# Optimization experiments

Hardware: AMD Instinct MI355X
Metric: run time of the kernel (lower is better)

Reference implementation:

```python
import jax, jax.numpy as jnp
import numpy as np

B, T, L = 4096, 26, 4      # batch, num sparse tables, bag size (multi-hot)
N_ROWS, M = 100000, 64     # rows per table, embedding dim
LN_BOT = [13, 512, 256, 64]
LN_TOP = [415, 512, 256, 1]


def _mlp_params(key, ln):
    Ws, bs = [], []
    for i in range(len(ln) - 1):
        n, m = ln[i], ln[i + 1]
        key, k1, k2 = jax.random.split(key, 3)
        Ws.append(jax.random.normal(k1, (m, n), jnp.float32) * np.sqrt(2.0 / (m + n)))
        bs.append(jax.random.normal(k2, (m,), jnp.float32) * np.sqrt(1.0 / m))
    return Ws, bs


def setup_inputs() -> dict:
    key = jax.random.key(0)
    k_dense, k_idx, k_emb, k_bot, k_top = jax.random.split(key, 5)
    dense_x = jax.random.normal(k_dense, (B, LN_BOT[0]), jnp.float32)
    sparse_idx = jax.random.randint(k_idx, (B, T, L), 0, N_ROWS, jnp.int64 if jax.config.jax_enable_x64 else jnp.int32)
    # per-table uniform init U(-1/sqrt(n), 1/sqrt(n)); all tables same size -> stacked
    bound = np.sqrt(1.0 / N_ROWS)
    emb_tables = jax.random.uniform(k_emb, (T, N_ROWS, M), jnp.float32, -bound, bound)
    bw, bb = _mlp_params(k_bot, LN_BOT)
    tw, tb = _mlp_params(k_top, LN_TOP)
    return {
        "dense_x": dense_x, "sparse_idx": sparse_idx, "emb_tables": emb_tables,
        "bot_W0": bw[0], "bot_b0": bb[0], "bot_W1": bw[1], "bot_b1": bb[1],
        "bot_W2": bw[2], "bot_b2": bb[2],
        "top_W0": tw[0], "top_b0": tb[0], "top_W1": tw[1], "top_b1": tb[1],
        "top_W2": tw[2], "top_b2": tb[2],
    }


def _dlrm_forward(dense_x, sparse_idx, emb_tables, bot, top):
    # bottom MLP (all ReLU; sigmoid_layer index not hit for bottom)
    x = dense_x
    for W, b in bot:
        x = jax.nn.relu(x @ W.T + b)                       # [B, 64] at the end
    # apply_emb: per-table EmbeddingBag(mode='sum'): gather L rows, sum-pool
    # emb_tables: [T, N, M], sparse_idx: [B, T, L] -> E: [B, T, M]
    E = jax.vmap(lambda tab, ix: tab[ix].sum(axis=1), in_axes=(0, 1), out_axes=1)(
        emb_tables, sparse_idx)
    # dot interaction: concat bottom output with pooled embeddings
    Tcat = jnp.concatenate([x[:, None, :], E], axis=1)     # [B, T+1, M]
    Z = jnp.einsum("bim,bjm->bij", Tcat, Tcat)             # [B, T+1, T+1]
    li, lj = np.tril_indices(T + 1, k=-1)                  # strictly lower triangle
    Zflat = Z[:, li, lj]                                   # [B, (T+1)T/2]
    R = jnp.concatenate([x, Zflat], axis=1)                # [B, 415]
    # top MLP: ReLU hidden, Sigmoid on last layer
    h = R
    for i, (W, b) in enumerate(top):
        h = h @ W.T + b
        h = jax.nn.sigmoid(h) if i == len(top) - 1 else jax.nn.relu(h)
    return h                                               # [B, 1]


def reference(dense_x, sparse_idx, emb_tables,
              bot_W0, bot_b0, bot_W1, bot_b1, bot_W2, bot_b2,
              top_W0, top_b0, top_W1, top_b1, top_W2, top_b2):
    bot = [(bot_W0, bot_b0), (bot_W1, bot_b1), (bot_W2, bot_b2)]
    top = [(top_W0, top_b0), (top_W1, top_b1), (top_W2, top_b2)]
    return _dlrm_forward(dense_x, sparse_idx, emb_tables, bot, top)
```

## Files before the change

kernel.cpp:

```cpp
#include <hip/hip_runtime.h>
#include <hip/hip_bf16.h>
#include <cstddef>
#include <cstdint>

#define BATCH 4096
#define TT 26
#define LL 4
#define NROWS 100000
#define MM 64
#define RSTR 512

typedef __attribute__((ext_vector_type(8))) short bf16x8;
typedef __attribute__((ext_vector_type(4))) float f32x4;

#define AS1 __attribute__((address_space(1)))
#define AS3 __attribute__((address_space(3)))

__device__ __forceinline__ void gload_lds16(const void* g, void* l) {
    __builtin_amdgcn_global_load_lds((const AS1 unsigned int*)g,
                                     (AS3 unsigned int*)l, 16, 0, 0);
}

__device__ __forceinline__ float bu2f(unsigned short u) {
    unsigned int x = (unsigned int)u << 16;
    float f; __builtin_memcpy(&f, &x, 4); return f;
}

#define CONV_BLOCKS 2112
__global__ __launch_bounds__(256) void prep_kernel(
    const float* __restrict__ dense, const float* __restrict__ bw0,
    const float* __restrict__ bb0,
    const float* __restrict__ bw1, const float* __restrict__ bw2,
    const float* __restrict__ tw0, const float* __restrict__ tw1,
    __hip_bfloat16* __restrict__ x1,
    __hip_bfloat16* __restrict__ bw1b, __hip_bfloat16* __restrict__ bw2b,
    __hip_bfloat16* __restrict__ tw0b, __hip_bfloat16* __restrict__ tw1b)
{
    __shared__ float xr[13];
    if (blockIdx.x < CONV_BLOCKS) {
        int i = blockIdx.x * 256 + threadIdx.x;
        if (i < 131072) {
            bw1b[i] = __float2bfloat16(bw1[i]);
        } else if (i < 147456) {
            int j = i - 131072; bw2b[j] = __float2bfloat16(bw2[j]);
        } else if (i < 409600) {
            int j = i - 147456; int n = j >> 9, k = j & 511;
            tw0b[j] = __float2bfloat16(k < 415 ? tw0[n * 415 + k] : 0.f);
        } else {
            int j = i - 409600; tw1b[j] = __float2bfloat16(tw1[j]);
        }
        return;
    }
    int b = blockIdx.x - CONV_BLOCKS;
    if (threadIdx.x < 13) xr[threadIdx.x] = dense[b * 13 + threadIdx.x];
    __syncthreads();
    for (int j = threadIdx.x; j < 512; j += 256) {
        const float* w = bw0 + j * 13;
        float s = bb0[j];
#pragma unroll
        for (int k = 0; k < 13; k++) s = fmaf(xr[k], w[k], s);
        x1[(size_t)b * 512 + j] = __float2bfloat16(fmaxf(s, 0.f));
    }
}

template<int KK, int ACT>
__global__ __launch_bounds__(256) void gemm_fullk(
    const __hip_bfloat16* __restrict__ A,
    const __hip_bfloat16* __restrict__ W,
    const float* __restrict__ bias,
    __hip_bfloat16* __restrict__ C, int ldc)
{
    constexpr int HS   = KK / 2;
    constexpr int CPRH = KK / 16;
    constexpr int NI   = (64 * CPRH) / 256;
    __shared__ __align__(16) short As0[64 * HS];
    __shared__ __align__(16) short As1[64 * HS];
    __shared__ __align__(16) short Bs0[64 * HS];
    __shared__ __align__(16) short Bs1[64 * HS];

    const int tid  = threadIdx.x;
    const int lane = tid & 63;
    const int wid  = tid >> 6;
    const int wr   = wid >> 1, wc = wid & 1;

    const char* Ab = (const char*)A + (size_t)blockIdx.x * (64 * KK * 2);
    const char* Wb = (const char*)W + (size_t)blockIdx.y * (64 * KK * 2);

    auto stage = [&](const char* Gb, short* Ls, int h) {
#pragma unroll
        for (int j = 0; j < NI; j++) {
            int ci  = j * 256 + tid;
            int row = ci / CPRH;
            int cb  = (ci & (CPRH - 1)) * 16;
            int src = row * (2 * KK) + h * KK + (cb ^ ((row & 7) << 4));
            gload_lds16(Gb + src, (char*)Ls + row * KK + cb);
        }
    };
    stage(Ab, As0, 0); stage(Wb, Bs0, 0);
    stage(Ab, As1, 1); stage(Wb, Bs1, 1);

    const int frow = lane & 15;
    const int fkb  = (lane >> 4) * 16;
    const int xr   = (frow & 7) << 4;
    const int oA0  = (wr * 32 + frow) * KK;
    const int oA1  = oA0 + 16 * KK;
    const int oB0  = (wc * 32 + frow) * KK;
    const int oB1  = oB0 + 16 * KK;

    f32x4 acc[2][2] = {};

    auto compute = [&](const short* Ah, const short* Bh) {
#pragma unroll
        for (int ks = 0; ks < KK / 64; ks++) {
            int pc = (ks * 64 + fkb) ^ xr;
            bf16x8 a0 = *(const bf16x8*)((const char*)Ah + oA0 + pc);
            bf16x8 a1 = *(const bf16x8*)((const char*)Ah + oA1 + pc);
            bf16x8 b0 = *(const bf16x8*)((const char*)Bh + oB0 + pc);
            bf16x8 b1 = *(const bf16x8*)((const char*)Bh + oB1 + pc);
            acc[0][0] = __builtin_amdgcn_mfma_f32_16x16x32_bf16(a0, b0, acc[0][0], 0, 0, 0);
            acc[0][1] = __builtin_amdgcn_mfma_f32_16x16x32_bf16(a0, b1, acc[0][1], 0, 0, 0);
            acc[1][0] = __builtin_amdgcn_mfma_f32_16x16x32_bf16(a1, b0, acc[1][0], 0, 0, 0);
            acc[1][1] = __builtin_amdgcn_mfma_f32_16x16x32_bf16(a1, b1, acc[1][1], 0, 0, 0);
        }
    };

    asm volatile("s_waitcnt vmcnt(%0)" :: "i"(2 * NI) : "memory");
    __builtin_amdgcn_sched_barrier(0);
    __builtin_amdgcn_s_barrier();
    __builtin_amdgcn_sched_barrier(0);
    compute(As0, Bs0);
    asm volatile("s_waitcnt vmcnt(0)" ::: "memory");
    __builtin_amdgcn_sched_barrier(0);
    __builtin_amdgcn_s_barrier();
    __builtin_amdgcn_sched_barrier(0);
    compute(As1, Bs1);

    const int col0 = blockIdx.y * 64 + wc * 32 + (lane & 15);
    const int row0 = blockIdx.x * 64 + wr * 32 + (lane >> 4) * 4;
    float bias_n0 = bias[col0];
    float bias_n1 = bias[col0 + 16];
#pragma unroll
    for (int mi = 0; mi < 2; mi++) {
#pragma unroll
        for (int j = 0; j < 4; j++) {
            int row = row0 + mi * 16 + j;
            float v0 = acc[mi][0][j] + bias_n0;
            float v1 = acc[mi][1][j] + bias_n1;
            if (ACT == 1) { v0 = fmaxf(v0, 0.f); v1 = fmaxf(v1, 0.f); }
            C[(size_t)row * ldc + col0]      = __float2bfloat16(v0);
            C[(size_t)row * ldc + col0 + 16] = __float2bfloat16(v1);
        }
    }
}

__global__ __launch_bounds__(256) void embed_interact_kernel(
    const int* __restrict__ idx, const float* __restrict__ emb,
    __hip_bfloat16* __restrict__ R)
{
    __shared__ float S[27 * 68];
    __shared__ int sidx[TT * LL];
    const int b = blockIdx.x;
    const int tid = threadIdx.x;
    const int lane = tid & 63;
    const int wid = tid >> 6;

    if (tid < TT * LL) sidx[tid] = idx[(size_t)b * (TT * LL) + tid];
    __syncthreads();

    float v[7][4];
#pragma unroll
    for (int rr = 0; rr < 7; rr++) {
        const int r = rr * 4 + wid;
        if (r == 0) {
            v[rr][0] = __bfloat162float(R[(size_t)b * RSTR + lane]);
            v[rr][1] = 0.f; v[rr][2] = 0.f; v[rr][3] = 0.f;
        } else if (r < 27) {
            const int t = r - 1;
            const float* tab = emb + (size_t)t * NROWS * MM;
#pragma unroll
            for (int l = 0; l < LL; l++)
                v[rr][l] = tab[(size_t)sidx[t * LL + l] * MM + lane];
        }
    }
#pragma unroll
    for (int rr = 0; rr < 7; rr++) {
        const int r = rr * 4 + wid;
        if (r < 27) S[r * 68 + lane] = v[rr][0] + v[rr][1] + v[rr][2] + v[rr][3];
    }
    __syncthreads();

    __hip_bfloat16* Rb = R + (size_t)b * RSTR;
    if (tid < 97) Rb[415 + tid] = __float2bfloat16(0.f);
    for (int e = tid; e < 351; e += 256) {
        int i = (int)((1.0f + sqrtf(1.0f + 8.0f * (float)e)) * 0.5f);
        while (i * (i - 1) / 2 > e) i--;
        while ((i + 1) * i / 2 <= e) i++;
        int j = e - i * (i - 1) / 2;
        const float* si_ = &S[i * 68];
        const float* sj_ = &S[j * 68];
        float s = 0.f;
#pragma unroll
        for (int k = 0; k < 16; k++) {
            float4 a  = *(const float4*)&si_[k * 4];
            float4 c4 = *(const float4*)&sj_[k * 4];
            s += a.x * c4.x + a.y * c4.y + a.z * c4.z + a.w * c4.w;
        }
        Rb[64 + e] = __float2bfloat16(s);
    }
}

__global__ __launch_bounds__(256) void top2_kernel(
    const __hip_bfloat16* __restrict__ h, const float* __restrict__ W,
    const float* __restrict__ bias, float* __restrict__ out)
{
    __shared__ float ws[256];
    int tid = threadIdx.x;
    ws[tid] = W[tid];
    __syncthreads();
    int b = blockIdx.x * 4 + (tid >> 6);
    int lane = tid & 63;
    const unsigned short* hb = (const unsigned short*)(h + (size_t)b * 256);
    ushort4 hv = *(const ushort4*)&hb[lane * 4];
    float4 wv = *(const float4*)&ws[lane * 4];
    float s = bu2f(hv.x) * wv.x + bu2f(hv.y) * wv.y + bu2f(hv.z) * wv.z + bu2f(hv.w) * wv.w;
#pragma unroll
    for (int off = 32; off >= 1; off >>= 1)
        s += __shfl_xor(s, off, 64);
    if (lane == 0) {
        float v = s + bias[0];
        out[b] = 1.0f / (1.0f + expf(-v));
    }
}

extern "C" void kernel_launch(void* const* d_in, const int* in_sizes, int n_in,
                              void* d_out, int out_size, void* d_ws, size_t ws_size,
                              hipStream_t stream) {
    const float* dense = (const float*)d_in[0];
    const int*   sidx  = (const int*)d_in[1];
    const float* emb   = (const float*)d_in[2];
    const float* bw0   = (const float*)d_in[3];
    const float* bb0   = (const float*)d_in[4];
    const float* bw1   = (const float*)d_in[5];
    const float* bb1   = (const float*)d_in[6];
    const float* bw2   = (const float*)d_in[7];
    const float* bb2   = (const float*)d_in[8];
    const float* tw0   = (const float*)d_in[9];
    const float* tb0   = (const float*)d_in[10];
    const float* tw1   = (const float*)d_in[11];
    const float* tb1   = (const float*)d_in[12];
    const float* tw2   = (const float*)d_in[13];
    const float* tb2   = (const float*)d_in[14];
    float* out = (float*)d_out;

    char* wsb = (char*)d_ws;
    __hip_bfloat16* x1   = (__hip_bfloat16*)(wsb);
    __hip_bfloat16* x2   = (__hip_bfloat16*)(wsb + (4u << 20));
    __hip_bfloat16* R    = (__hip_bfloat16*)(wsb + (8u << 20));
    __hip_bfloat16* h1   = (__hip_bfloat16*)(wsb + (12u << 20));
    __hip_bfloat16* h2   = (__hip_bfloat16*)(wsb + (16u << 20));
    __hip_bfloat16* bw1b = (__hip_bfloat16*)(wsb + (18u << 20));
    __hip_bfloat16* bw2b = bw1b + 131072;
    __hip_bfloat16* tw0b = bw2b + 16384;
    __hip_bfloat16* tw1b = tw0b + 262144;

    prep_kernel<<<CONV_BLOCKS + BATCH, 256, 0, stream>>>(
        dense, bw0, bb0, bw1, bw2, tw0, tw1, x1, bw1b, bw2b, tw0b, tw1b);

    gemm_fullk<512, 1><<<dim3(64, 4), 256, 0, stream>>>(x1, bw1b, bb1, x2, 256);

    gemm_fullk<256, 1><<<dim3(64, 1), 256, 0, stream>>>(x2, bw2b, bb2, R, RSTR);

    embed_interact_kernel<<<BATCH, 256, 0, stream>>>(sidx, emb, R);

    gemm_fullk<512, 1><<<dim3(64, 8), 256, 0, stream>>>(R, tw0b, tb0, h1, 512);

    gemm_fullk<512, 1><<<dim3(64, 4), 256, 0, stream>>>(h1, tw1b, tb1, h2, 256);

    top2_kernel<<<BATCH / 4, 256, 0, stream>>>(h2, tw2, tb2, out);
}
```

Measured before the change: 55.66 us.

## Fuse bottom MLP last layer into embedding gather and MFMA interaction kernel

Removes the separate last bottom-MLP GEMM launch by computing it inside the embedding kernel with 16x16x32 bf16 MFMA for 4 batch rows per block. Each wave now handles one sample, storing pooled embeddings as bf16 in a swizzled LDS tile, and computes the 27x27 Gram matrix with 32x32x16 MFMAs instead of scalar dot products with triangular index decoding. This saves a launch and the scalar interaction work, but rounds pooled embeddings to bf16 before the dot products. The MFMA operand mapping for the tiny GEMM (only 4 real rows in a 16-row tile) wastes lanes.

```diff
diff --git a/kernel.cpp b/kernel.cpp
--- a/kernel.cpp
+++ b/kernel.cpp
@@ -12,6 +12,7 @@
 
 typedef __attribute__((ext_vector_type(8))) short bf16x8;
 typedef __attribute__((ext_vector_type(4))) float f32x4;
+typedef __attribute__((ext_vector_type(16))) float f32x16;
 
 #define AS1 __attribute__((address_space(1)))
 #define AS3 __attribute__((address_space(3)))
@@ -153,59 +154,88 @@
     }
 }
 
-__global__ __launch_bounds__(256) void embed_interact_kernel(
+__global__ __launch_bounds__(256) void bot2_embed_interact(
     const int* __restrict__ idx, const float* __restrict__ emb,
-    __hip_bfloat16* __restrict__ R)
+    const __hip_bfloat16* __restrict__ x2, const __hip_bfloat16* __restrict__ w2b,
+    const float* __restrict__ bb2, __hip_bfloat16* __restrict__ R)
 {
-    __shared__ float S[27 * 68];
-    __shared__ int sidx[TT * LL];
-    const int b = blockIdx.x;
-    const int tid = threadIdx.x;
+    __shared__ __align__(16) short T[4][32 * 64];
+    __shared__ int sidx[4 * TT * LL];
+    const int tid  = threadIdx.x;
     const int lane = tid & 63;
-    const int wid = tid >> 6;
-
-    if (tid < TT * LL) sidx[tid] = idx[(size_t)b * (TT * LL) + tid];
+    const int w    = tid >> 6;
+    const int b0   = blockIdx.x * 4;
+
+    for (int i = tid; i < 4 * TT * LL; i += 256)
+        sidx[i] = idx[(size_t)b0 * (TT * LL) + i];
+
+    {
+        f32x4 acc = {};
+        const short* xg = (const short*)x2 + (size_t)(b0 + (lane & 3)) * 256 + (lane >> 4) * 8;
+        const short* wg = (const short*)w2b + (size_t)(w * 16 + (lane & 15)) * 256 + (lane >> 4) * 8;
+#pragma unroll
+        for (int ks = 0; ks < 8; ks++) {
+            bf16x8 a  = *(const bf16x8*)(xg + ks * 32);
+            bf16x8 bf = *(const bf16x8*)(wg + ks * 32);
+            acc = __builtin_amdgcn_mfma_f32_16x16x32_bf16(a, bf, acc, 0, 0, 0);
+        }
+        __syncthreads();
+        if (lane < 16) {
+            int col = w * 16 + lane;
+            float bias = bb2[col];
+#pragma unroll
+            for (int j = 0; j < 4; j++) {
+                float v = fmaxf(acc[j] + bias, 0.f);
+                __hip_bfloat16 hv = __float2bfloat16(v);
+                R[(size_t)(b0 + j) * RSTR + col] = hv;
+                T[j][col] = *(short*)&hv;
+            }
+        }
+    }
+
+#pragma unroll
+    for (int r = 27; r < 32; r++) {
+        int byteoff = r * 128 + ((lane * 2) ^ ((r & 7) << 4));
+        *(short*)((char*)T[w] + byteoff) = 0;
+    }
+
+#pragma unroll
+    for (int t = 0; t < TT; t++) {
+        const float* tab = emb + (size_t)t * NROWS * MM + lane;
+        const int* ip = &sidx[(w * TT + t) * LL];
+        float s = tab[(size_t)ip[0] * MM] + tab[(size_t)ip[1] * MM]
+                + tab[(size_t)ip[2] * MM] + tab[(size_t)ip[3] * MM];
+        __hip_bfloat16 hv = __float2bfloat16(s);
+        int r = t + 1;
+        int byteoff = r * 128 + ((lane * 2) ^ ((r & 7) << 4));
+        *(short*)((char*)T[w] + byteoff) = *(short*)&hv;
+    }
     __syncthreads();
 
-    float v[7][4];
-#pragma unroll
-    for (int rr = 0; rr < 7; rr++) {
-        const int r = rr * 4 + wid;
-        if (r == 0) {
-            v[rr][0] = __bfloat162float(R[(size_t)b * RSTR + lane]);
-            v[rr][1] = 0.f; v[rr][2] = 0.f; v[rr][3] = 0.f;
-        } else if (r < 27) {
-            const int t = r - 1;
-            const float* tab = emb + (size_t)t * NROWS * MM;
-#pragma unroll
-            for (int l = 0; l < LL; l++)
-                v[rr][l] = tab[(size_t)sidx[t * LL + l] * MM + lane];
-        }
-    }
-#pragma unroll
-    for (int rr = 0; rr < 7; rr++) {
-        const int r = rr * 4 + wid;
-        if (r < 27) S[r * 68 + lane] = v[rr][0] + v[rr][1] + v[rr][2] + v[rr][3];
-    }
-    __syncthreads();
-
-    __hip_bfloat16* Rb = R + (size_t)b * RSTR;
-    if (tid < 97) Rb[415 + tid] = __float2bfloat16(0.f);
-    for (int e = tid; e < 351; e += 256) {
-        int i = (int)((1.0f + sqrtf(1.0f + 8.0f * (float)e)) * 0.5f);
-        while (i * (i - 1) / 2 > e) i--;
-        while ((i + 1) * i / 2 <= e) i++;
-        int j = e - i * (i - 1) / 2;
-        const float* si_ = &S[i * 68];
-        const float* sj_ = &S[j * 68];
-        float s = 0.f;
-#pragma unroll
-        for (int k = 0; k < 16; k++) {
-            float4 a  = *(const float4*)&si_[k * 4];
-            float4 c4 = *(const float4*)&sj_[k * 4];
-            s += a.x * c4.x + a.y * c4.y + a.z * c4.z + a.w * c4.w;
-        }
-        Rb[64 + e] = __float2bfloat16(s);
+    {
+        f32x16 acc = {};
+#pragma unroll
+        for (int m = 0; m < 4; m++) {
+            int byteoff = (lane & 31) * 128 +
+                          ((m * 32 + (lane >> 5) * 16) ^ (((lane & 31) & 7) << 4));
+            bf16x8 f = *(const bf16x8*)((const char*)T[w] + byteoff);
+            acc = __builtin_amdgcn_mfma_f32_32x32x16_bf16(f, f, acc, 0, 0, 0);
+        }
+        __hip_bfloat16* Rb = R + (size_t)(b0 + w) * RSTR;
+        const int col = lane & 31;
+#pragma unroll
+        for (int q = 0; q < 4; q++) {
+#pragma unroll
+            for (int j = 0; j < 4; j++) {
+                int row = j + 8 * q + 4 * (lane >> 5);
+                if (row < 27 && col < row) {
+                    int e = row * (row - 1) / 2 + col;
+                    Rb[64 + e] = __float2bfloat16(acc[q * 4 + j]);
+                }
+            }
+        }
+        for (int p = lane; p < 97; p += 64)
+            Rb[415 + p] = __float2bfloat16(0.f);
     }
 }
 
@@ -268,9 +298,7 @@
 
     gemm_fullk<512, 1><<<dim3(64, 4), 256, 0, stream>>>(x1, bw1b, bb1, x2, 256);
 
-    gemm_fullk<256, 1><<<dim3(64, 1), 256, 0, stream>>>(x2, bw2b, bb2, R, RSTR);
-
-    embed_interact_kernel<<<BATCH, 256, 0, stream>>>(sidx, emb, R);
+    bot2_embed_interact<<<BATCH / 4, 256, 0, stream>>>(sidx, emb, x2, bw2b, bb2, R);
 
     gemm_fullk<512, 1><<<dim3(64, 8), 256, 0, stream>>>(R, tw0b, tb0, h1, 512);
 
```

After: 63.64 us. 1.14x slower.

## Compute embedding dot interactions with a single-wave bf16 MFMA Gram matrix

Applied to the files above, without the earlier changes.

Pooled embeddings are stored to LDS as bf16 in a XOR-swizzled 32x64 tile, with padding rows zeroed. One wavefront then computes the full 32x32 Gram matrix with four 32x32x16 bf16 MFMAs and writes out the strictly lower triangle. This replaces the per-thread scalar fp32 dot products and the triangular index search. It lowers the precision of the interaction inputs to bf16, and only one wave does the interaction while the other three sit idle.

```diff
diff --git a/kernel.cpp b/kernel.cpp
--- a/kernel.cpp
+++ b/kernel.cpp
@@ -12,6 +12,7 @@
 
 typedef __attribute__((ext_vector_type(8))) short bf16x8;
 typedef __attribute__((ext_vector_type(4))) float f32x4;
+typedef __attribute__((ext_vector_type(16))) float f32x16;
 
 #define AS1 __attribute__((address_space(1)))
 #define AS3 __attribute__((address_space(3)))
@@ -157,55 +158,70 @@
     const int* __restrict__ idx, const float* __restrict__ emb,
     __hip_bfloat16* __restrict__ R)
 {
-    __shared__ float S[27 * 68];
+    __shared__ __align__(16) short T[32 * 64];
     __shared__ int sidx[TT * LL];
     const int b = blockIdx.x;
     const int tid = threadIdx.x;
     const int lane = tid & 63;
-    const int wid = tid >> 6;
+    const int w = tid >> 6;
 
     if (tid < TT * LL) sidx[tid] = idx[(size_t)b * (TT * LL) + tid];
+    for (int i = tid; i < 5 * 64; i += 256) {
+        int r = 27 + (i >> 6), l = i & 63;
+        *(short*)((char*)T + r * 128 + ((l * 2) ^ ((r & 7) << 4))) = 0;
+    }
     __syncthreads();
 
     float v[7][4];
 #pragma unroll
     for (int rr = 0; rr < 7; rr++) {
-        const int r = rr * 4 + wid;
+        const int r = rr * 4 + w;
         if (r == 0) {
             v[rr][0] = __bfloat162float(R[(size_t)b * RSTR + lane]);
             v[rr][1] = 0.f; v[rr][2] = 0.f; v[rr][3] = 0.f;
         } else if (r < 27) {
             const int t = r - 1;
-            const float* tab = emb + (size_t)t * NROWS * MM;
+            const float* tab = emb + (size_t)t * NROWS * MM + lane;
 #pragma unroll
             for (int l = 0; l < LL; l++)
-                v[rr][l] = tab[(size_t)sidx[t * LL + l] * MM + lane];
+                v[rr][l] = tab[(size_t)sidx[t * LL + l] * MM];
         }
     }
 #pragma unroll
     for (int rr = 0; rr < 7; rr++) {
-        const int r = rr * 4 + wid;
-        if (r < 27) S[r * 68 + lane] = v[rr][0] + v[rr][1] + v[rr][2] + v[rr][3];
+        const int r = rr * 4 + w;
+        if (r < 27) {
+            float s = v[rr][0] + v[rr][1] + v[rr][2] + v[rr][3];
+            __hip_bfloat16 hv = __float2bfloat16(s);
+            *(short*)((char*)T + r * 128 + ((lane * 2) ^ ((r & 7) << 4))) = *(short*)&hv;
+        }
     }
     __syncthreads();
 
     __hip_bfloat16* Rb = R + (size_t)b * RSTR;
-    if (tid < 97) Rb[415 + tid] = __float2bfloat16(0.f);
-    for (int e = tid; e < 351; e += 256) {
-        int i = (int)((1.0f + sqrtf(1.0f + 8.0f * (float)e)) * 0.5f);
-        while (i * (i - 1) / 2 > e) i--;
-        while ((i + 1) * i / 2 <= e) i++;
-        int j = e - i * (i - 1) / 2;
-        const float* si_ = &S[i * 68];
-        const float* sj_ = &S[j * 68];
-        float s = 0.f;
-#pragma unroll
-        for (int k = 0; k < 16; k++) {
-            float4 a  = *(const float4*)&si_[k * 4];
-            float4 c4 = *(const float4*)&sj_[k * 4];
-            s += a.x * c4.x + a.y * c4.y + a.z * c4.z + a.w * c4.w;
-        }
-        Rb[64 + e] = __float2bfloat16(s);
+    if (w == 1) {
+        Rb[415 + lane] = __float2bfloat16(0.f);
+        if (lane < 33) Rb[479 + lane] = __float2bfloat16(0.f);
+    }
+    if (w == 0) {
+        f32x16 acc = {};
+#pragma unroll
+        for (int m = 0; m < 4; m++) {
+            int byteoff = (lane & 31) * 128 +
+                          ((m * 32 + (lane >> 5) * 16) ^ ((lane & 7) << 4));
+            bf16x8 f = *(const bf16x8*)((const char*)T + byteoff);
+            acc = __builtin_amdgcn_mfma_f32_32x32x16_bf16(f, f, acc, 0, 0, 0);
+        }
+        const int col = lane & 31;
+#pragma unroll
+        for (int q = 0; q < 4; q++) {
+#pragma unroll
+            for (int j = 0; j < 4; j++) {
+                int row = j + 8 * q + 4 * (lane >> 5);
+                if (row < 27 && col < row)
+                    Rb[64 + row * (row - 1) / 2 + col] = __float2bfloat16(acc[q * 4 + j]);
+            }
+        }
     }
 }
 
```

Result: no change. 54.66 us (-1.8%).
